# Performance work log

Measured on AMD Instinct MI355X. Metric: run time of the kernel, lower is better.

Reference implementation:

```python
import jax, jax.numpy as jnp
import numpy as np
from jax import lax

GRID = 200      # _FIXED_GRID_LEN
SOFT_K = 50.0   # _SOFT_MASK_K
BN_EPS = 1e-5


def setup_inputs() -> dict:
    key = jax.random.key(0)
    ks = jax.random.split(key, 12)
    B, L = 8192, 2001
    f32 = jnp.float32
    inp = {
        'phase': jax.random.uniform(ks[0], (B, L), f32, -1.0, 1.0),
        'primary_flux': 0.01 * jax.random.normal(ks[1], (B, L), f32),
        'secondary_flux': 0.01 * jax.random.normal(ks[2], (B, L), f32),
        'odd_even_diff': 0.01 * jax.random.normal(ks[3], (B, L), f32),
        # TaylorGateLayerV8 params
        'A': jnp.asarray(0.01, f32),
        'Bp': jnp.asarray(1.0, f32),
        't0': jnp.asarray(0.0, f32),
        # BatchNorm1d(4), eval mode (running stats)
        'bn_gamma': jnp.ones((4,), f32),
        'bn_beta': jnp.zeros((4,), f32),
        'bn_mean': jnp.zeros((4,), f32),
        'bn_var': jnp.ones((4,), f32),
        # Conv1d(4,8,7) / Conv1d(8,16,5)
        'conv1_w': 0.1 * jax.random.normal(ks[4], (8, 4, 7), f32),
        'conv1_b': jnp.zeros((8,), f32),
        'conv2_w': 0.1 * jax.random.normal(ks[5], (16, 8, 5), f32),
        'conv2_b': jnp.zeros((16,), f32),
        # Linear(21, 1)
        'fc_w': 0.1 * jax.random.normal(ks[6], (1, 21), f32),
        'fc_b': jnp.zeros((1,), f32),
    }
    return inp


def _conv1d(x, w, b, pad):
    # x: (B, C, L), w: (O, C, K)
    y = lax.conv_general_dilated(x, w, window_strides=(1,), padding=[(pad, pad)],
                                 dimension_numbers=('NCH', 'OIH', 'NCH'))
    return y + b[None, :, None]


def _interp_linear_ac(x, out_len):
    # torch F.interpolate(mode='linear', align_corners=True) on (B, L) -> (B, out_len)
    L = x.shape[1]
    pos = jnp.linspace(0.0, L - 1.0, out_len)
    i0 = jnp.floor(pos).astype(jnp.int32)
    i1 = jnp.minimum(i0 + 1, L - 1)
    w = (pos - i0).astype(x.dtype)
    return x[:, i0] * (1.0 - w) + x[:, i1] * w


def reference(phase, primary_flux, secondary_flux, odd_even_diff,
              A, Bp, t0, bn_gamma, bn_beta, bn_mean, bn_var,
              conv1_w, conv1_b, conv2_w, conv2_b, fc_w, fc_b):
    # --- TaylorGateLayerV8: 2nd-order Taylor U-shape transit template ---
    gate = -A * jnp.clip(1.0 - Bp * (phase - t0) ** 2, 0.0, None)

    # --- CNN branch ---
    x = jnp.stack([gate, primary_flux, secondary_flux, odd_even_diff], axis=1)  # (B,4,L)
    inv = bn_gamma / jnp.sqrt(bn_var + BN_EPS)
    x = x * inv[None, :, None] + (bn_beta - bn_mean * inv)[None, :, None]
    x = jax.nn.relu(_conv1d(x, conv1_w, conv1_b, 3))
    x = jax.nn.relu(_conv1d(x, conv2_w, conv2_b, 2))
    cnn_out = jnp.mean(x, axis=2)  # AdaptiveAvgPool1d(1) -> (B,16)

    # --- shape features ---
    batch = primary_flux.shape[0]
    A_abs = jnp.abs(A) + 1e-8
    depth = jnp.clip(-primary_flux, 0.0, None)
    depth_norm = depth / A_abs
    depth_rs = _interp_linear_ac(depth, GRID)  # (B, 200)
    dx = 2.0 / (GRID - 1)                       # trapz over linspace(-1,1,200)
    auc_raw = dx * (jnp.sum(depth_rs, axis=1) - 0.5 * (depth_rs[:, 0] + depth_rs[:, -1]))
    auc_norm = auc_raw / A_abs
    dip_all = jax.nn.sigmoid(SOFT_K * (depth_norm - 0.1))
    flat_bot = jax.nn.sigmoid(SOFT_K * (depth_norm - 0.8))
    ingress = dip_all - flat_bot
    total = 1.0 - dip_all + ingress + flat_bot + 1e-8
    ingress = ingress / total
    flat_bot = flat_bot / total
    t14 = jnp.mean(ingress + flat_bot, axis=1) + 1e-8
    t12_t14 = jnp.mean(ingress, axis=1) / t14
    flat_bottom = jnp.mean(flat_bot, axis=1)
    B_bcast = jnp.broadcast_to(Bp, (batch,)).astype(depth.dtype)
    shape = jnp.stack([B_bcast, auc_raw, auc_norm, t12_t14, flat_bottom], axis=1)  # (B,5)

    features = jnp.concatenate([cnn_out, shape], axis=1)  # (B,21)
    logits = features @ fc_w.T + fc_b
    return jax.nn.sigmoid(logits)
```

## Files before the change

### kernel.cpp

```cpp
#include <hip/hip_runtime.h>
#include <math.h>

#define L_LEN 2001
#define CCH 1024
#define XREC 1056

typedef __attribute__((ext_vector_type(8))) short bf16x8;
typedef __attribute__((ext_vector_type(4))) float f32x4;
#if __has_builtin(__builtin_amdgcn_cvt_pk_bf16_f32)
typedef __attribute__((ext_vector_type(2))) __bf16 bf16x2_t;
#endif

union FragU { unsigned u[4]; uint2 u2[2]; uint4 u4; bf16x8 v; };

__device__ __forceinline__ unsigned short f2bf(float f) {
    unsigned u = __builtin_bit_cast(unsigned, f);
    u += 0x7fffu + ((u >> 16) & 1u);
    return (unsigned short)(u >> 16);
}
__device__ __forceinline__ unsigned bfpack(float lo, float hi) {
#if __has_builtin(__builtin_amdgcn_cvt_pk_bf16_f32)
    bf16x2_t r = __builtin_amdgcn_cvt_pk_bf16_f32(lo, hi);
    return __builtin_bit_cast(unsigned, r);
#else
    unsigned ul = __builtin_bit_cast(unsigned, lo);
    unsigned uh = __builtin_bit_cast(unsigned, hi);
    ul += 0x7fffu + ((ul >> 16) & 1u);
    uh += 0x7fffu + ((uh >> 16) & 1u);
    return __builtin_amdgcn_perm(uh, ul, 0x07060302);
#endif
}
__device__ __forceinline__ float fast_rcp(float x) { return __builtin_amdgcn_rcpf(x); }
__device__ __forceinline__ float fexp2(float x) {
#if __has_builtin(__builtin_amdgcn_exp2f)
    return __builtin_amdgcn_exp2f(x);
#else
    return __expf(x * 0.69314718f);
#endif
}

__global__ __launch_bounds__(256, 6)
void taylor_cnn_v8_mfma(const float* __restrict__ phase, const float* __restrict__ primary,
                        const float* __restrict__ secondary, const float* __restrict__ oddeven,
                        const float* __restrict__ pA, const float* __restrict__ pBp,
                        const float* __restrict__ pT0,
                        const float* __restrict__ bng, const float* __restrict__ bnb,
                        const float* __restrict__ bnm, const float* __restrict__ bnv,
                        const float* __restrict__ w1, const float* __restrict__ b1,
                        const float* __restrict__ w2, const float* __restrict__ b2,
                        const float* __restrict__ fcw, const float* __restrict__ fcb,
                        float* __restrict__ out, int nrows)
{
    __shared__ __align__(16) unsigned int xs_i[XREC * 2];
    __shared__ __align__(16) unsigned int y1_i[XREC * 4];
    __shared__ float redA[4][16];
    __shared__ float redB[4][3];

    const int tid = threadIdx.x;
    const int row = blockIdx.x;
    const long base = (long)row * L_LEN;

    const int lane = tid & 63;
    const int wid  = tid >> 6;
    const int n    = lane & 15;
    const int quad = lane >> 4;

    const float A  = pA[0];
    const float Bp = pBp[0];
    const float t0 = pT0[0];
    const float A_abs = fabsf(A) + 1e-8f;
    const float rAabs = 1.0f / A_abs;
    const float nBp  = -Bp;
    const float cExp = -72.134766f * rAabs;

    float inv1, inv2, inv3, gInv0, off0, off1, off2, off3;
    {
        float iv0 = bng[0] / sqrtf(bnv[0] + 1e-5f);
        float iv1 = bng[1] / sqrtf(bnv[1] + 1e-5f);
        float iv2 = bng[2] / sqrtf(bnv[2] + 1e-5f);
        float iv3 = bng[3] / sqrtf(bnv[3] + 1e-5f);
        gInv0 = -A * iv0;
        inv1 = iv1; inv2 = iv2; inv3 = iv3;
        off0 = bnb[0] - bnm[0] * iv0;
        off1 = bnb[1] - bnm[1] * iv1;
        off2 = bnb[2] - bnm[2] * iv2;
        off3 = bnb[3] - bnm[3] * iv3;
    }

    bf16x8 a1;
#pragma unroll
    for (int jp = 0; jp < 8; ++jp) {
        int j = quad + 4 * (jp >> 2);
        int c = jp & 3;
        float v = (n < 8 && j < 7) ? w1[(n * 4 + c) * 7 + j] : 0.0f;
        a1[jp] = (short)f2bf(v);
    }
    bf16x8 a20, a21;
#pragma unroll
    for (int jp = 0; jp < 8; ++jp) {
        float v0 = w2[(n * 8 + jp) * 5 + quad];
        float v1 = (quad + 4 < 5) ? w2[(n * 8 + jp) * 5 + quad + 4] : 0.0f;
        a20[jp] = (short)f2bf(v0);
        a21[jp] = (short)f2bf(v1);
    }
    f32x4 cb1, cb2;
#pragma unroll
    for (int r = 0; r < 4; ++r) {
        cb1[r] = b1[(quad * 4 + r) & 7];
        cb2[r] = b2[quad * 4 + r];
    }

    float s_ing = 0.0f, s_fb = 0.0f;
    float m0 = 0.f, m1 = 0.f, m2 = 0.f, m3 = 0.f;

    float s_auc = 0.0f;
    if (tid < 200) {
        float pos = (float)tid * (2000.0f / 199.0f);
        int i0 = (int)pos;
        if (i0 > 2000) i0 = 2000;
        int i1 = (i0 + 1 < L_LEN) ? i0 + 1 : 2000;
        float w  = pos - (float)i0;
        float d0 = fmaxf(-primary[base + i0], 0.f);
        float d1 = fmaxf(-primary[base + i1], 0.f);
        float v  = d0 * (1.0f - w) + d1 * w;
        float wt = (tid == 0 || tid == 199) ? 0.5f : 1.0f;
        s_auc = v * wt;
    }

    auto aRec = [&](int m, int p, bool chk) {
        bool valid = true, core = true;
        int pc = p;
        if (chk) {
            valid = ((unsigned)p < (unsigned)L_LEN);
            core  = valid && (m >= 16) && (m < 16 + CCH);
            pc = min(max(p, 0), L_LEN - 1);
        }
        float ph = phase[base + pc];
        float pf = primary[base + pc];
        float sf = secondary[base + pc];
        float oe = oddeven[base + pc];
        float dd = ph - t0;
        float g  = fmaxf(fmaf(dd * dd, nBp, 1.0f), 0.0f);
        float x0 = fmaf(g,  gInv0, off0);
        float x1 = fmaf(pf, inv1, off1);
        float x2 = fmaf(sf, inv2, off2);
        float x3 = fmaf(oe, inv3, off3);
        unsigned d0 = bfpack(x0, x1);
        unsigned d1 = bfpack(x2, x3);
        if (chk && !valid) { d0 = 0u; d1 = 0u; }
        *(uint2*)&xs_i[2 * m] = make_uint2(d0, d1);
        float depth = fmaxf(-pf, 0.0f);
        float e   = fexp2(depth * cExp);
        float dip = fast_rcp(fmaf(e, 148.413159f, 1.0f));
        float fb  = fast_rcp(fmaf(e, 2.35385267e17f, 1.0f));
        float ing = dip - fb;
        if (chk && !core) { ing = 0.f; fb = 0.f; }
        s_ing += ing;
        s_fb  += fb;
    };

    auto stageA0 = [&]() {
        aRec(tid, tid - 16, true);
#pragma unroll
        for (int k = 1; k < 4; ++k) aRec(tid + 256 * k, tid + 256 * k - 16, false);
        if (tid < 32) aRec(1024 + tid, 1008 + tid, true);
    };
    auto stageA1 = [&]() {
        aRec(tid, 1008 + tid, true);
#pragma unroll
        for (int k = 1; k < 3; ++k) aRec(tid + 256 * k, 1008 + tid + 256 * k, false);
        aRec(tid + 768, 1776 + tid, true);
    };

    auto stageB = [&](int c0, int nt, int straddle_t) {
        for (int t = wid; t < nt; t += 4) {
            int qb = 16 * t + n + quad + 5;
            FragU bu;
            bu.u2[0] = *(const uint2*)&xs_i[2 * qb];
            bu.u2[1] = *(const uint2*)&xs_i[2 * (qb + 4)];
            f32x4 d = __builtin_amdgcn_mfma_f32_16x16x32_bf16(a1, bu.v, cb1, 0, 0, 0);
            if (lane < 32) {
                int q = 16 * t + n;
                unsigned w0, w1_;
                if (t == straddle_t) {
                    int p = c0 - 8 + q;
                    bool ok = ((unsigned)p < (unsigned)L_LEN);
                    w0  = ok ? bfpack(fmaxf(d[0], 0.f), fmaxf(d[1], 0.f)) : 0u;
                    w1_ = ok ? bfpack(fmaxf(d[2], 0.f), fmaxf(d[3], 0.f)) : 0u;
                } else {
                    w0  = bfpack(fmaxf(d[0], 0.f), fmaxf(d[1], 0.f));
                    w1_ = bfpack(fmaxf(d[2], 0.f), fmaxf(d[3], 0.f));
                }
                *(uint2*)&y1_i[4 * q + 2 * quad] = make_uint2(w0, w1_);
            }
        }
    };

    auto stageC = [&](int nt, bool maskLast) {
        for (int t = wid; t < nt; t += 4) {
            int q = 16 * t + n + quad + 6;
            FragU u0, u1;
            u0.u4 = *(const uint4*)&y1_i[4 * q];
            u1.u4 = *(const uint4*)&y1_i[4 * (q + 4)];
            f32x4 d = __builtin_amdgcn_mfma_f32_16x16x32_bf16(a20, u0.v, cb2, 0, 0, 0);
            d = __builtin_amdgcn_mfma_f32_16x16x32_bf16(a21, u1.v, d, 0, 0, 0);
            if (maskLast && t == 61) {
                float msk = (n == 0) ? 1.0f : 0.0f;
                m0 = fmaf(fmaxf(d[0], 0.f), msk, m0);
                m1 = fmaf(fmaxf(d[1], 0.f), msk, m1);
                m2 = fmaf(fmaxf(d[2], 0.f), msk, m2);
                m3 = fmaf(fmaxf(d[3], 0.f), msk, m3);
            } else {
                m0 += fmaxf(d[0], 0.f);
                m1 += fmaxf(d[1], 0.f);
                m2 += fmaxf(d[2], 0.f);
                m3 += fmaxf(d[3], 0.f);
            }
        }
    };

    stageA0();
    __syncthreads();
    stageB(0, 65, 0);
    __syncthreads();
    stageA1();
    stageC(64, false);
    __syncthreads();
    stageB(1024, 62, 61);
    __syncthreads();
    stageC(62, true);

#pragma unroll
    for (int dlt = 8; dlt >= 1; dlt >>= 1) {
        m0 += __shfl_xor(m0, dlt);
        m1 += __shfl_xor(m1, dlt);
        m2 += __shfl_xor(m2, dlt);
        m3 += __shfl_xor(m3, dlt);
    }
    if ((lane & 15) == 0) {
        redA[wid][quad * 4 + 0] = m0;
        redA[wid][quad * 4 + 1] = m1;
        redA[wid][quad * 4 + 2] = m2;
        redA[wid][quad * 4 + 3] = m3;
    }
#pragma unroll
    for (int dlt = 32; dlt >= 1; dlt >>= 1) {
        s_ing += __shfl_xor(s_ing, dlt);
        s_fb  += __shfl_xor(s_fb,  dlt);
        s_auc += __shfl_xor(s_auc, dlt);
    }
    if (lane == 0) {
        redB[wid][0] = s_ing;
        redB[wid][1] = s_fb;
        redB[wid][2] = s_auc;
    }
    __syncthreads();

    if (tid == 0) {
        float logit = fcb[0];
#pragma unroll
        for (int oc = 0; oc < 16; ++oc) {
            float s = redA[0][oc] + redA[1][oc] + redA[2][oc] + redA[3][oc];
            logit += (s / 2001.0f) * fcw[oc];
        }
        float Sing = redB[0][0] + redB[1][0] + redB[2][0] + redB[3][0];
        float Sfb  = redB[0][1] + redB[1][1] + redB[2][1] + redB[3][1];
        float Sauc = redB[0][2] + redB[1][2] + redB[2][2] + redB[3][2];

        float auc_raw  = (float)(2.0 / 199.0) * Sauc;
        float auc_norm = auc_raw / A_abs;
        float m_ing = Sing / 2001.0f;
        float m_fb  = Sfb  / 2001.0f;
        float t14   = (Sing + Sfb) / 2001.0f + 1e-8f;
        float t12   = m_ing / t14;

        logit += Bp       * fcw[16]
               + auc_raw  * fcw[17]
               + auc_norm * fcw[18]
               + t12      * fcw[19]
               + m_fb     * fcw[20];

        out[row] = 1.0f / (1.0f + expf(-logit));
    }
}

extern "C" void kernel_launch(void* const* d_in, const int* in_sizes, int n_in,
                              void* d_out, int out_size, void* d_ws, size_t ws_size,
                              hipStream_t stream) {
    const float* phase     = (const float*)d_in[0];
    const float* primary   = (const float*)d_in[1];
    const float* secondary = (const float*)d_in[2];
    const float* oddeven   = (const float*)d_in[3];
    const float* pA        = (const float*)d_in[4];
    const float* pBp       = (const float*)d_in[5];
    const float* pT0       = (const float*)d_in[6];
    const float* bng       = (const float*)d_in[7];
    const float* bnb       = (const float*)d_in[8];
    const float* bnm       = (const float*)d_in[9];
    const float* bnv       = (const float*)d_in[10];
    const float* w1        = (const float*)d_in[11];
    const float* b1        = (const float*)d_in[12];
    const float* w2        = (const float*)d_in[13];
    const float* b2        = (const float*)d_in[14];
    const float* fcw       = (const float*)d_in[15];
    const float* fcb       = (const float*)d_in[16];
    float* out = (float*)d_out;

    int nrows = in_sizes[0] / L_LEN;
    dim3 grid(nrows), block(256);
    hipLaunchKernelGGL(taylor_cnn_v8_mfma, grid, block, 0, stream,
                       phase, primary, secondary, oddeven, pA, pBp, pT0,
                       bng, bnb, bnm, bnv, w1, b1, w2, b2, fcw, fcb, out, nrows);
}
```

Measured before the change: 305.3 us.

## Split row processing into three smaller LDS chunks to raise occupancy

Result: slower. 320.5 us (+5.0%).

```diff
diff --git a/kernel.cpp b/kernel.cpp
--- a/kernel.cpp
+++ b/kernel.cpp
@@ -2,8 +2,10 @@
 #include <math.h>
 
 #define L_LEN 2001
-#define CCH 1024
-#define XREC 1056
+#define CCH 672
+#define XR  704
+#define NTB 43
+#define NTC 42
 
 typedef __attribute__((ext_vector_type(8))) short bf16x8;
 typedef __attribute__((ext_vector_type(4))) float f32x4;
@@ -39,7 +41,7 @@
 #endif
 }
 
-__global__ __launch_bounds__(256, 6)
+__global__ __launch_bounds__(256, 8)
 void taylor_cnn_v8_mfma(const float* __restrict__ phase, const float* __restrict__ primary,
                         const float* __restrict__ secondary, const float* __restrict__ oddeven,
                         const float* __restrict__ pA, const float* __restrict__ pBp,
@@ -51,14 +53,15 @@
                         const float* __restrict__ fcw, const float* __restrict__ fcb,
                         float* __restrict__ out, int nrows)
 {
-    __shared__ __align__(16) unsigned int xs_i[XREC * 2];
-    __shared__ __align__(16) unsigned int y1_i[XREC * 4];
+    __shared__ __align__(16) unsigned int xs_i[XR * 2];
+    __shared__ __align__(16) unsigned int y1_i[XR * 4];
     __shared__ float redA[4][16];
     __shared__ float redB[4][3];
 
     const int tid = threadIdx.x;
     const int row = blockIdx.x;
     const long base = (long)row * L_LEN;
+    (void)nrows;
 
     const int lane = tid & 63;
     const int wid  = tid >> 6;
@@ -159,21 +162,15 @@
         s_fb  += fb;
     };
 
-    auto stageA0 = [&]() {
-        aRec(tid, tid - 16, true);
-#pragma unroll
-        for (int k = 1; k < 4; ++k) aRec(tid + 256 * k, tid + 256 * k - 16, false);
-        if (tid < 32) aRec(1024 + tid, 1008 + tid, true);
+    auto stageA = [&](int c0) {
+        const int pb = c0 - 16;
+        aRec(tid,       pb + tid,       true);
+        aRec(tid + 256, pb + tid + 256, false);
+        if (tid < 192) aRec(tid + 512, pb + tid + 512, true);
     };
-    auto stageA1 = [&]() {
-        aRec(tid, 1008 + tid, true);
-#pragma unroll
-        for (int k = 1; k < 3; ++k) aRec(tid + 256 * k, 1008 + tid + 256 * k, false);
-        aRec(tid + 768, 1776 + tid, true);
-    };
-
-    auto stageB = [&](int c0, int nt, int straddle_t) {
-        for (int t = wid; t < nt; t += 4) {
+
+    auto stageB = [&](int c0, int tLo, int tFrom) {
+        for (int t = wid; t < NTB; t += 4) {
             int qb = 16 * t + n + quad + 5;
             FragU bu;
             bu.u2[0] = *(const uint2*)&xs_i[2 * qb];
@@ -182,7 +179,7 @@
             if (lane < 32) {
                 int q = 16 * t + n;
                 unsigned w0, w1_;
-                if (t == straddle_t) {
+                if (t == tLo || t >= tFrom) {
                     int p = c0 - 8 + q;
                     bool ok = ((unsigned)p < (unsigned)L_LEN);
                     w0  = ok ? bfpack(fmaxf(d[0], 0.f), fmaxf(d[1], 0.f)) : 0u;
@@ -196,15 +193,15 @@
         }
     };
 
-    auto stageC = [&](int nt, bool maskLast) {
-        for (int t = wid; t < nt; t += 4) {
+    auto stageC = [&](int maskT) {
+        for (int t = wid; t < NTC; t += 4) {
             int q = 16 * t + n + quad + 6;
             FragU u0, u1;
             u0.u4 = *(const uint4*)&y1_i[4 * q];
             u1.u4 = *(const uint4*)&y1_i[4 * (q + 4)];
             f32x4 d = __builtin_amdgcn_mfma_f32_16x16x32_bf16(a20, u0.v, cb2, 0, 0, 0);
             d = __builtin_amdgcn_mfma_f32_16x16x32_bf16(a21, u1.v, d, 0, 0, 0);
-            if (maskLast && t == 61) {
+            if (t == maskT) {
                 float msk = (n == 0) ? 1.0f : 0.0f;
                 m0 = fmaf(fmaxf(d[0], 0.f), msk, m0);
                 m1 = fmaf(fmaxf(d[1], 0.f), msk, m1);
@@ -219,16 +216,21 @@
         }
     };
 
-    stageA0();
-    __syncthreads();
-    stageB(0, 65, 0);
-    __syncthreads();
-    stageA1();
-    stageC(64, false);
-    __syncthreads();
-    stageB(1024, 62, 61);
-    __syncthreads();
-    stageC(62, true);
+    stageA(0);
+    __syncthreads();
+    stageB(0, 0, 99);
+    __syncthreads();
+    stageA(CCH);
+    stageC(-1);
+    __syncthreads();
+    stageB(CCH, -1, 99);
+    __syncthreads();
+    stageA(2 * CCH);
+    stageC(-1);
+    __syncthreads();
+    stageB(2 * CCH, -1, 41);
+    __syncthreads();
+    stageC(41);
 
 #pragma unroll
     for (int dlt = 8; dlt >= 1; dlt >>= 1) {
```
